# Kernel tuning notes

Measured on AMD Instinct MI355X. Metric: run time of the kernel, lower is better.

Reference implementation:

```python
import jax, jax.numpy as jnp
import numpy as np

NUM_HEADS = 16
HIDDEN = 1024
HEAD_DIM = HIDDEN // NUM_HEADS


def setup_inputs() -> dict:
    key = jax.random.key(0)
    ks = jax.random.split(key, 9)
    B, S = 2, 2048
    s = 1.0 / np.sqrt(HIDDEN)
    return {
        "x": jax.random.normal(ks[0], (B, S, HIDDEN), dtype=jnp.float32),
        "Wq": jax.random.normal(ks[1], (HIDDEN, HIDDEN), dtype=jnp.float32) * s,
        "bq": jnp.zeros((HIDDEN,), dtype=jnp.float32),
        "Wk": jax.random.normal(ks[2], (HIDDEN, HIDDEN), dtype=jnp.float32) * s,
        "bk": jnp.zeros((HIDDEN,), dtype=jnp.float32),
        "Wv": jax.random.normal(ks[3], (HIDDEN, HIDDEN), dtype=jnp.float32) * s,
        "bv": jnp.zeros((HIDDEN,), dtype=jnp.float32),
        "Wo": jax.random.normal(ks[4], (HIDDEN, HIDDEN), dtype=jnp.float32) * s,
        "bo": jnp.zeros((HIDDEN,), dtype=jnp.float32),
    }


def reference(x, Wq, bq, Wk, bk, Wv, bv, Wo, bo):
    B, S, H = x.shape
    # project and split heads: [B, S, H] -> [B, nh, S, hd]
    def split_heads(t):
        return t.reshape(B, S, NUM_HEADS, HEAD_DIM).transpose(0, 2, 1, 3)

    q = split_heads(x @ Wq + bq)
    k = split_heads(x @ Wk + bk)
    v = split_heads(x @ Wv + bv)

    scores = jnp.einsum("bhqd,bhkd->bhqk", q, k) / jnp.sqrt(
        jnp.asarray(HEAD_DIM, dtype=x.dtype))
    probs = jax.nn.softmax(scores, axis=-1)
    # attn_drop_rate = 0.0 -> dropout is identity
    ctx = jnp.einsum("bhqk,bhkd->bhqd", probs, v)
    ctx = ctx.transpose(0, 2, 1, 3).reshape(B, S, H)
    out = ctx @ Wo + bo
    return out
```

## Files before the change

### kernel.cpp

```cpp
#include <hip/hip_runtime.h>

#define NHEADS 16
#define HDIM   64
#define SEQL   2048
#define HID    1024
#define NB     2
#define MT     4096

#define QSCALE 0.18033688011112042f

typedef float        f4_t   __attribute__((ext_vector_type(4)));
typedef unsigned int u32x4  __attribute__((ext_vector_type(4)));
typedef __bf16       bf16x8 __attribute__((ext_vector_type(8)));

typedef const __attribute__((address_space(1))) unsigned int* gas_ptr;
typedef __attribute__((address_space(3))) unsigned int*       las_ptr;

__device__ __forceinline__ void gload16(const void* g, void* l){
  __builtin_amdgcn_global_load_lds((gas_ptr)g, (las_ptr)l, 16, 0, 0);
}
__device__ __forceinline__ unsigned int pkbf(float a, float b){
  unsigned short lo = __builtin_bit_cast(unsigned short, (__bf16)a);
  unsigned short hi = __builtin_bit_cast(unsigned short, (__bf16)b);
  return (unsigned)lo | ((unsigned)hi << 16);
}
__device__ __forceinline__ unsigned short f2bf(float f){
  return __builtin_bit_cast(unsigned short, (__bf16)f);
}
__device__ __forceinline__ u32x4 ld16(const unsigned short* p){
  return *reinterpret_cast<const u32x4*>(p);
}
__device__ __forceinline__ f4_t mfma_bf16(u32x4 a, u32x4 b, f4_t c){
  return __builtin_amdgcn_mfma_f32_16x16x32_bf16(
      __builtin_bit_cast(bf16x8, a), __builtin_bit_cast(bf16x8, b), c, 0, 0, 0);
}

__global__ __launch_bounds__(256) void xcast(const float* __restrict__ x,
                                             unsigned short* __restrict__ xb){
  int gid = blockIdx.x * 256 + threadIdx.x;
  float4 a = reinterpret_cast<const float4*>(x)[gid * 2];
  float4 b = reinterpret_cast<const float4*>(x)[gid * 2 + 1];
  u32x4 o;
  o[0] = pkbf(a.x, a.y);
  o[1] = pkbf(a.z, a.w);
  o[2] = pkbf(b.x, b.y);
  o[3] = pkbf(b.z, b.w);
  *reinterpret_cast<u32x4*>(&xb[gid * 8]) = o;
}

__global__ void prep_w(const float* __restrict__ Wq, const float* __restrict__ Wk,
                       const float* __restrict__ Wv, const float* __restrict__ Wo,
                       unsigned short* __restrict__ wqT, unsigned short* __restrict__ wkT,
                       unsigned short* __restrict__ wvT, unsigned short* __restrict__ woT){
  __shared__ float t[32][33];
  int z = blockIdx.z;
  const float* W = (z==0)?Wq:(z==1)?Wk:(z==2)?Wv:Wo;
  unsigned short* WT = (z==0)?wqT:(z==1)?wkT:(z==2)?wvT:woT;
  float sc = (z==0) ? QSCALE : 1.0f;
  int k0 = blockIdx.x*32, n0 = blockIdx.y*32;
  int tx = threadIdx.x, ty = threadIdx.y;
  #pragma unroll
  for (int ii=0; ii<4; ii++)
    t[ty+ii*8][tx] = W[(k0+ty+ii*8)*HID + n0+tx];
  __syncthreads();
  #pragma unroll
  for (int ii=0; ii<4; ii++)
    WT[(n0+ty+ii*8)*HID + k0+tx] = f2bf(t[tx][ty+ii*8] * sc);
}

__global__ __launch_bounds__(256) void qkv_gemm(
    const unsigned short* __restrict__ xb,
    const unsigned short* __restrict__ wqT, const unsigned short* __restrict__ wkT,
    const unsigned short* __restrict__ wvT,
    const float* __restrict__ bq, const float* __restrict__ bk, const float* __restrict__ bv,
    unsigned short* __restrict__ qo, unsigned short* __restrict__ ko,
    unsigned short* __restrict__ vto){
  __shared__ unsigned short As[128*32];
  __shared__ unsigned short Bs[128*32];
  const int z = blockIdx.z;
  const unsigned short* wT = (z==0)?wqT:(z==1)?wkT:wvT;
  const float* bias = (z==0)?bq:(z==1)?bk:bv;
  const float bscale = (z==0) ? QSCALE : 1.0f;
  const int m0 = blockIdx.x * 128;
  const int n0 = blockIdx.y * 128;
  const int tid = threadIdx.x;
  const int lane = tid & 63, w = tid >> 6;
  const int l15 = lane & 15, lg = lane >> 4;
  const int wr = (w >> 1) * 64, wc = (w & 1) * 64;
  const int srow = w*16 + (lane >> 2);
  const int skc  = (lane & 3) * 8;

  f4_t acc[4][4];
  f4_t z4 = {0.f, 0.f, 0.f, 0.f};
  #pragma unroll
  for (int i=0;i<4;i++)
    #pragma unroll
    for (int j=0;j<4;j++) acc[i][j] = z4;

  for (int kt = 0; kt < HID; kt += 32) {
    __syncthreads();
    #pragma unroll
    for (int c = 0; c < 2; c++) {
      int row = c*64 + srow;
      gload16(&xb[(m0+row)*HID + kt + skc], (char*)As + c*4096 + w*1024);
      gload16(&wT[(n0+row)*HID + kt + skc], (char*)Bs + c*4096 + w*1024);
    }
    __syncthreads();
    u32x4 a[4], b[4];
    #pragma unroll
    for (int i=0;i<4;i++) a[i] = ld16(&As[(wr + i*16 + l15)*32 + lg*8]);
    #pragma unroll
    for (int j=0;j<4;j++) b[j] = ld16(&Bs[(wc + j*16 + l15)*32 + lg*8]);
    #pragma unroll
    for (int i=0;i<4;i++)
      #pragma unroll
      for (int j=0;j<4;j++)
        acc[i][j] = mfma_bf16(a[i], b[j], acc[i][j]);
  }
  if (z == 2) {
    #pragma unroll
    for (int i=0;i<4;i++){
      int mrow = m0 + wr + i*16 + lg*4;
      int b_ = mrow >> 11, s = mrow & 2047;
      #pragma unroll
      for (int j=0;j<4;j++){
        int n = n0 + wc + j*16 + l15;
        float bs = bias[n];
        int h = n >> 6, d = n & 63;
        unsigned int lo = pkbf(acc[i][j][0]+bs, acc[i][j][1]+bs);
        unsigned int hi = pkbf(acc[i][j][2]+bs, acc[i][j][3]+bs);
        unsigned long long v8 = (unsigned long long)lo | ((unsigned long long)hi << 32);
        *reinterpret_cast<unsigned long long*>(
            vto + (((b_*NHEADS + h)*HDIM + d)*SEQL + s)) = v8;
      }
    }
  } else {
    unsigned short* outp = (z==0) ? qo : ko;
    #pragma unroll
    for (int i=0;i<4;i++){
      int mrow = m0 + wr + i*16 + lg*4;
      #pragma unroll
      for (int j=0;j<4;j++){
        int n = n0 + wc + j*16 + l15;
        float bs = bias[n] * bscale;
        int h = n >> 6, d = n & 63;
        #pragma unroll
        for (int r=0;r<4;r++){
          int m = mrow + r;
          int b_ = m >> 11, s = m & 2047;
          outp[(((b_*NHEADS + h)*SEQL) + s)*HDIM + d] = f2bf(acc[i][j][r] + bs);
        }
      }
    }
  }
}

__global__ __launch_bounds__(256) void flash(
    const unsigned short* __restrict__ q,
    const unsigned short* __restrict__ k,
    const unsigned short* __restrict__ vT,
    unsigned short* __restrict__ ctx){
  __shared__ unsigned short Ks[2][4096];
  __shared__ unsigned short Vs[2][4096];
  __shared__ unsigned short Ps[4][2048];
  const int bh = blockIdx.y;
  const int b_ = bh >> 4, h = bh & 15;
  const int tid = threadIdx.x;
  const int w = tid >> 6, lane = tid & 63;
  const int l15 = lane & 15, lg = lane >> 4;
  const int q0 = blockIdx.x*128 + w*32;
  const unsigned short* qb = q + (bh*SEQL + q0)*HDIM;
  const unsigned short* kp = k + bh*SEQL*HDIM;
  const unsigned short* vp = vT + bh*HDIM*SEQL;
  char* pw = (char*)Ps[w];
  const int swz = (l15 & 7) << 4;

  const int sr = w*16 + (lane >> 3);
  const int scol = ((lane & 7) ^ (sr & 7)) * 8;
  const int ldst = w*2048;

  u32x4 qf[2][2];
  #pragma unroll
  for (int qg=0; qg<2; qg++)
    #pragma unroll
    for (int ks=0; ks<2; ks++)
      qf[qg][ks] = ld16(&qb[(qg*16 + l15)*HDIM + ks*32 + lg*8]);

  float mr[2] = {-1e30f, -1e30f}, ls[2] = {0.f, 0.f};
  f4_t oacc[4][2];
  f4_t z4 = {0.f,0.f,0.f,0.f};
  #pragma unroll
  for (int dt=0;dt<4;dt++)
    #pragma unroll
    for (int qg=0;qg<2;qg++) oacc[dt][qg] = z4;

  auto stage = [&](int buf, int kb){
    const unsigned short* gk = kp + (kb + sr)*HDIM + scol;
    gload16(gk,           (char*)Ks[buf] + ldst);
    gload16(gk + 8*HDIM,  (char*)Ks[buf] + ldst + 1024);
    const unsigned short* gv = vp + sr*SEQL + kb + scol;
    gload16(gv,           (char*)Vs[buf] + ldst);
    gload16(gv + 8*SEQL,  (char*)Vs[buf] + ldst + 1024);
  };

  int cur = 0;
  stage(0, 0);
  __syncthreads();

  for (int kb = 0; kb < SEQL; kb += 64) {
    if (kb + 64 < SEQL) stage(cur^1, kb + 64);
    const char* kbase = (const char*)Ks[cur];
    const char* vbase = (const char*)Vs[cur];

    f4_t sacc[4][2];
    __builtin_amdgcn_s_setprio(1);
    #pragma unroll
    for (int t=0;t<4;t++){
      u32x4 k0 = *reinterpret_cast<const u32x4*>(kbase + (t*16+l15)*128 + ((lg*16) ^ swz));
      u32x4 k1 = *reinterpret_cast<const u32x4*>(kbase + (t*16+l15)*128 + ((64 + lg*16) ^ swz));
      #pragma unroll
      for (int qg=0;qg<2;qg++){
        f4_t s = mfma_bf16(k0, qf[qg][0], z4);
        sacc[t][qg] = mfma_bf16(k1, qf[qg][1], s);
      }
    }
    __builtin_amdgcn_s_setprio(0);

    float scl[2];
    #pragma unroll
    for (int qg=0;qg<2;qg++){
      float vm = sacc[0][qg][0];
      #pragma unroll
      for (int t=0;t<4;t++)
        #pragma unroll
        for (int r=0;r<4;r++) vm = fmaxf(vm, sacc[t][qg][r]);
      vm = fmaxf(vm, __shfl_xor(vm, 16));
      vm = fmaxf(vm, __shfl_xor(vm, 32));
      float mnew = fmaxf(mr[qg], vm);
      scl[qg] = exp2f(mr[qg] - mnew);
      mr[qg] = mnew;
      float ps = 0.f;
      #pragma unroll
      for (int t=0;t<4;t++)
        #pragma unroll
        for (int r=0;r<4;r++){
          float p = exp2f(sacc[t][qg][r] - mnew);
          sacc[t][qg][r] = p;
          ps += p;
        }
      ps += __shfl_xor(ps, 16);
      ps += __shfl_xor(ps, 32);
      ls[qg] = ls[qg]*scl[qg] + ps;
      int rowb = (qg*16 + l15)*128;
      #pragma unroll
      for (int t=0;t<4;t++){
        unsigned int lo = pkbf(sacc[t][qg][0], sacc[t][qg][1]);
        unsigned int hi = pkbf(sacc[t][qg][2], sacc[t][qg][3]);
        unsigned long long v8 = (unsigned long long)lo | ((unsigned long long)hi << 32);
        *reinterpret_cast<unsigned long long*>(pw + rowb + ((t*32 + lg*8) ^ swz)) = v8;
      }
    }
    #pragma unroll
    for (int dt=0;dt<4;dt++)
      #pragma unroll
      for (int qg=0;qg<2;qg++) oacc[dt][qg] *= scl[qg];

    u32x4 pf[2][2];
    #pragma unroll
    for (int qg=0;qg<2;qg++)
      #pragma unroll
      for (int ks=0;ks<2;ks++)
        pf[qg][ks] = *reinterpret_cast<const u32x4*>(
            pw + (qg*16 + l15)*128 + ((ks*64 + lg*16) ^ swz));

    __builtin_amdgcn_s_setprio(1);
    #pragma unroll
    for (int dt=0;dt<4;dt++){
      u32x4 v0 = *reinterpret_cast<const u32x4*>(vbase + (dt*16+l15)*128 + ((lg*16) ^ swz));
      u32x4 v1 = *reinterpret_cast<const u32x4*>(vbase + (dt*16+l15)*128 + ((64 + lg*16) ^ swz));
      #pragma unroll
      for (int qg=0;qg<2;qg++){
        f4_t o = mfma_bf16(v0, pf[qg][0], oacc[dt][qg]);
        oacc[dt][qg] = mfma_bf16(v1, pf[qg][1], o);
      }
    }
    __builtin_amdgcn_s_setprio(0);
    __syncthreads();
    cur ^= 1;
  }

  #pragma unroll
  for (int qg=0;qg<2;qg++){
    float inv = 1.0f / ls[qg];
    int orow = b_*SEQL + q0 + qg*16 + l15;
    unsigned short* cb = ctx + orow*HID + h*HDIM;
    #pragma unroll
    for (int dt=0;dt<4;dt++){
      unsigned int lo = pkbf(oacc[dt][qg][0]*inv, oacc[dt][qg][1]*inv);
      unsigned int hi = pkbf(oacc[dt][qg][2]*inv, oacc[dt][qg][3]*inv);
      unsigned long long v8 = (unsigned long long)lo | ((unsigned long long)hi << 32);
      *reinterpret_cast<unsigned long long*>(cb + dt*16 + lg*4) = v8;
    }
  }
}

__global__ __launch_bounds__(256) void out_gemm(
    const unsigned short* __restrict__ cb,
    const unsigned short* __restrict__ woT,
    const float* __restrict__ bo,
    float* __restrict__ out){
  __shared__ unsigned short As[128*32];
  __shared__ unsigned short Bs[128*32];
  const int m0 = blockIdx.x * 128;
  const int n0 = blockIdx.y * 128;
  const int tid = threadIdx.x;
  const int lane = tid & 63, w = tid >> 6;
  const int l15 = lane & 15, lg = lane >> 4;
  const int wr = (w >> 1) * 64, wc = (w & 1) * 64;
  const int srow = w*16 + (lane >> 2);
  const int skc  = (lane & 3) * 8;

  f4_t acc[4][4];
  f4_t z4 = {0.f,0.f,0.f,0.f};
  #pragma unroll
  for (int i=0;i<4;i++)
    #pragma unroll
    for (int j=0;j<4;j++) acc[i][j] = z4;

  for (int kt = 0; kt < HID; kt += 32) {
    __syncthreads();
    #pragma unroll
    for (int c = 0; c < 2; c++) {
      int row = c*64 + srow;
      gload16(&cb[(m0+row)*HID + kt + skc],  (char*)As + c*4096 + w*1024);
      gload16(&woT[(n0+row)*HID + kt + skc], (char*)Bs + c*4096 + w*1024);
    }
    __syncthreads();
    u32x4 a[4], b[4];
    #pragma unroll
    for (int i=0;i<4;i++) a[i] = ld16(&As[(wr + i*16 + l15)*32 + lg*8]);
    #pragma unroll
    for (int j=0;j<4;j++) b[j] = ld16(&Bs[(wc + j*16 + l15)*32 + lg*8]);
    #pragma unroll
    for (int i=0;i<4;i++)
      #pragma unroll
      for (int j=0;j<4;j++)
        acc[i][j] = mfma_bf16(a[i], b[j], acc[i][j]);
  }
  #pragma unroll
  for (int i=0;i<4;i++){
    int mrow = m0 + wr + i*16 + lg*4;
    #pragma unroll
    for (int j=0;j<4;j++){
      int n = n0 + wc + j*16 + l15;
      float bs = bo[n];
      #pragma unroll
      for (int r=0;r<4;r++)
        out[(mrow + r)*HID + n] = acc[i][j][r] + bs;
    }
  }
}

extern "C" void kernel_launch(void* const* d_in, const int* in_sizes, int n_in,
                              void* d_out, int out_size, void* d_ws, size_t ws_size,
                              hipStream_t stream){
  const float* x  = (const float*)d_in[0];
  const float* Wq = (const float*)d_in[1];
  const float* bq = (const float*)d_in[2];
  const float* Wk = (const float*)d_in[3];
  const float* bk = (const float*)d_in[4];
  const float* Wv = (const float*)d_in[5];
  const float* bv = (const float*)d_in[6];
  const float* Wo = (const float*)d_in[7];
  const float* bo = (const float*)d_in[8];
  float* out = (float*)d_out;

  char* ws = (char*)d_ws;
  size_t off = 0;
  auto alloc = [&](size_t bytes) -> void* {
    void* p = ws + off;
    off += (bytes + 255) & ~(size_t)255;
    return p;
  };
  unsigned short* xb   = (unsigned short*)alloc((size_t)MT*HID*2);
  unsigned short* wqT  = (unsigned short*)alloc((size_t)HID*HID*2);
  unsigned short* wkT  = (unsigned short*)alloc((size_t)HID*HID*2);
  unsigned short* wvT  = (unsigned short*)alloc((size_t)HID*HID*2);
  unsigned short* woT  = (unsigned short*)alloc((size_t)HID*HID*2);
  unsigned short* q_ws = (unsigned short*)alloc((size_t)MT*HID*2);
  unsigned short* k_ws = (unsigned short*)alloc((size_t)MT*HID*2);
  unsigned short* vT_ws= (unsigned short*)alloc((size_t)MT*HID*2);
  unsigned short* c_ws = (unsigned short*)alloc((size_t)MT*HID*2);

  prep_w<<<dim3(32,32,4), dim3(32,8), 0, stream>>>(Wq,Wk,Wv,Wo, wqT,wkT,wvT,woT);
  xcast<<<dim3(2048), dim3(256), 0, stream>>>(x, xb);
  qkv_gemm<<<dim3(32,8,3), dim3(256), 0, stream>>>(xb, wqT,wkT,wvT, bq,bk,bv,
                                                   q_ws, k_ws, vT_ws);
  flash<<<dim3(16,32), dim3(256), 0, stream>>>(q_ws, k_ws, vT_ws, c_ws);
  out_gemm<<<dim3(32,8), dim3(256), 0, stream>>>(c_ws, woT, bo, out);
}
```

Before: 177.8 us.

## Split flash attention across 8 waves with 16 rows each and lazy rescaling

The flash kernel now runs 512 threads per block, and each of 8 waves handles 16 query rows instead of 4 waves handling 32. That halves per-wave registers and accumulators and shares the K/V staging across more waves. It also adds a conditional online-softmax rescale: the running max and accumulators are only updated when a wave-wide new max exceeds the old one by more than a threshold. This trades exp and multiply work for more waves contending at each barrier, and risks larger exp values in bf16 P when rescaling is skipped.

```diff
diff --git a/kernel.cpp b/kernel.cpp
--- a/kernel.cpp
+++ b/kernel.cpp
@@ -8,6 +8,7 @@
 #define MT     4096
 
 #define QSCALE 0.18033688011112042f
+#define RESCALE_THR 6.0f
 
 typedef float        f4_t   __attribute__((ext_vector_type(4)));
 typedef unsigned int u32x4  __attribute__((ext_vector_type(4)));
@@ -155,52 +156,44 @@
   }
 }
 
-__global__ __launch_bounds__(256) void flash(
+__global__ __launch_bounds__(512) void flash(
     const unsigned short* __restrict__ q,
     const unsigned short* __restrict__ k,
     const unsigned short* __restrict__ vT,
     unsigned short* __restrict__ ctx){
   __shared__ unsigned short Ks[2][4096];
   __shared__ unsigned short Vs[2][4096];
-  __shared__ unsigned short Ps[4][2048];
+  __shared__ unsigned short Ps[8][1024];
   const int bh = blockIdx.y;
   const int b_ = bh >> 4, h = bh & 15;
   const int tid = threadIdx.x;
   const int w = tid >> 6, lane = tid & 63;
   const int l15 = lane & 15, lg = lane >> 4;
-  const int q0 = blockIdx.x*128 + w*32;
+  const int q0 = blockIdx.x*128 + w*16;
   const unsigned short* qb = q + (bh*SEQL + q0)*HDIM;
   const unsigned short* kp = k + bh*SEQL*HDIM;
   const unsigned short* vp = vT + bh*HDIM*SEQL;
   char* pw = (char*)Ps[w];
   const int swz = (l15 & 7) << 4;
 
-  const int sr = w*16 + (lane >> 3);
+  const int sr = w*8 + (lane >> 3);
   const int scol = ((lane & 7) ^ (sr & 7)) * 8;
-  const int ldst = w*2048;
-
-  u32x4 qf[2][2];
-  #pragma unroll
-  for (int qg=0; qg<2; qg++)
-    #pragma unroll
-    for (int ks=0; ks<2; ks++)
-      qf[qg][ks] = ld16(&qb[(qg*16 + l15)*HDIM + ks*32 + lg*8]);
-
-  float mr[2] = {-1e30f, -1e30f}, ls[2] = {0.f, 0.f};
-  f4_t oacc[4][2];
+  const int ldst = w*1024;
+
+  u32x4 qf[2];
+  #pragma unroll
+  for (int ks=0; ks<2; ks++)
+    qf[ks] = ld16(&qb[l15*HDIM + ks*32 + lg*8]);
+
+  float mr = -1e30f, ls = 0.f;
+  f4_t oacc[4];
   f4_t z4 = {0.f,0.f,0.f,0.f};
   #pragma unroll
-  for (int dt=0;dt<4;dt++)
-    #pragma unroll
-    for (int qg=0;qg<2;qg++) oacc[dt][qg] = z4;
+  for (int dt=0;dt<4;dt++) oacc[dt] = z4;
 
   auto stage = [&](int buf, int kb){
-    const unsigned short* gk = kp + (kb + sr)*HDIM + scol;
-    gload16(gk,           (char*)Ks[buf] + ldst);
-    gload16(gk + 8*HDIM,  (char*)Ks[buf] + ldst + 1024);
-    const unsigned short* gv = vp + sr*SEQL + kb + scol;
-    gload16(gv,           (char*)Vs[buf] + ldst);
-    gload16(gv + 8*SEQL,  (char*)Vs[buf] + ldst + 1024);
+    gload16(kp + (kb + sr)*HDIM + scol, (char*)Ks[buf] + ldst);
+    gload16(vp + sr*SEQL + kb + scol,   (char*)Vs[buf] + ldst);
   };
 
   int cur = 0;
@@ -212,95 +205,82 @@
     const char* kbase = (const char*)Ks[cur];
     const char* vbase = (const char*)Vs[cur];
 
-    f4_t sacc[4][2];
+    f4_t sacc[4];
     __builtin_amdgcn_s_setprio(1);
     #pragma unroll
     for (int t=0;t<4;t++){
       u32x4 k0 = *reinterpret_cast<const u32x4*>(kbase + (t*16+l15)*128 + ((lg*16) ^ swz));
       u32x4 k1 = *reinterpret_cast<const u32x4*>(kbase + (t*16+l15)*128 + ((64 + lg*16) ^ swz));
-      #pragma unroll
-      for (int qg=0;qg<2;qg++){
-        f4_t s = mfma_bf16(k0, qf[qg][0], z4);
-        sacc[t][qg] = mfma_bf16(k1, qf[qg][1], s);
+      f4_t s = mfma_bf16(k0, qf[0], z4);
+      sacc[t] = mfma_bf16(k1, qf[1], s);
+    }
+    __builtin_amdgcn_s_setprio(0);
+
+    float vm = sacc[0][0];
+    #pragma unroll
+    for (int t=0;t<4;t++)
+      #pragma unroll
+      for (int r=0;r<4;r++) vm = fmaxf(vm, sacc[t][r]);
+    vm = fmaxf(vm, __shfl_xor(vm, 16));
+    vm = fmaxf(vm, __shfl_xor(vm, 32));
+    if (!__all(vm - mr <= RESCALE_THR)) {
+      float mnew = fmaxf(mr, vm);
+      float scl = exp2f(mr - mnew);
+      mr = mnew;
+      ls *= scl;
+      #pragma unroll
+      for (int dt=0;dt<4;dt++) oacc[dt] *= scl;
+    }
+    float ps = 0.f;
+    #pragma unroll
+    for (int t=0;t<4;t++)
+      #pragma unroll
+      for (int r=0;r<4;r++){
+        float p = exp2f(sacc[t][r] - mr);
+        sacc[t][r] = p;
+        ps += p;
       }
-    }
-    __builtin_amdgcn_s_setprio(0);
-
-    float scl[2];
-    #pragma unroll
-    for (int qg=0;qg<2;qg++){
-      float vm = sacc[0][qg][0];
-      #pragma unroll
-      for (int t=0;t<4;t++)
-        #pragma unroll
-        for (int r=0;r<4;r++) vm = fmaxf(vm, sacc[t][qg][r]);
-      vm = fmaxf(vm, __shfl_xor(vm, 16));
-      vm = fmaxf(vm, __shfl_xor(vm, 32));
-      float mnew = fmaxf(mr[qg], vm);
-      scl[qg] = exp2f(mr[qg] - mnew);
-      mr[qg] = mnew;
-      float ps = 0.f;
-      #pragma unroll
-      for (int t=0;t<4;t++)
-        #pragma unroll
-        for (int r=0;r<4;r++){
-          float p = exp2f(sacc[t][qg][r] - mnew);
-          sacc[t][qg][r] = p;
-          ps += p;
-        }
-      ps += __shfl_xor(ps, 16);
-      ps += __shfl_xor(ps, 32);
-      ls[qg] = ls[qg]*scl[qg] + ps;
-      int rowb = (qg*16 + l15)*128;
+    ps += __shfl_xor(ps, 16);
+    ps += __shfl_xor(ps, 32);
+    ls += ps;
+    {
+      int rowb = l15*128;
       #pragma unroll
       for (int t=0;t<4;t++){
-        unsigned int lo = pkbf(sacc[t][qg][0], sacc[t][qg][1]);
-        unsigned int hi = pkbf(sacc[t][qg][2], sacc[t][qg][3]);
+        unsigned int lo = pkbf(sacc[t][0], sacc[t][1]);
+        unsigned int hi = pkbf(sacc[t][2], sacc[t][3]);
         unsigned long long v8 = (unsigned long long)lo | ((unsigned long long)hi << 32);
         *reinterpret_cast<unsigned long long*>(pw + rowb + ((t*32 + lg*8) ^ swz)) = v8;
       }
     }
-    #pragma unroll
-    for (int dt=0;dt<4;dt++)
-      #pragma unroll
-      for (int qg=0;qg<2;qg++) oacc[dt][qg] *= scl[qg];
-
-    u32x4 pf[2][2];
-    #pragma unroll
-    for (int qg=0;qg<2;qg++)
-      #pragma unroll
-      for (int ks=0;ks<2;ks++)
-        pf[qg][ks] = *reinterpret_cast<const u32x4*>(
-            pw + (qg*16 + l15)*128 + ((ks*64 + lg*16) ^ swz));
+    u32x4 pf[2];
+    #pragma unroll
+    for (int ks=0;ks<2;ks++)
+      pf[ks] = *reinterpret_cast<const u32x4*>(
+          pw + l15*128 + ((ks*64 + lg*16) ^ swz));
 
     __builtin_amdgcn_s_setprio(1);
     #pragma unroll
     for (int dt=0;dt<4;dt++){
       u32x4 v0 = *reinterpret_cast<const u32x4*>(vbase + (dt*16+l15)*128 + ((lg*16) ^ swz));
       u32x4 v1 = *reinterpret_cast<const u32x4*>(vbase + (dt*16+l15)*128 + ((64 + lg*16) ^ swz));
-      #pragma unroll
-      for (int qg=0;qg<2;qg++){
-        f4_t o = mfma_bf16(v0, pf[qg][0], oacc[dt][qg]);
-        oacc[dt][qg] = mfma_bf16(v1, pf[qg][1], o);
-      }
+      f4_t o = mfma_bf16(v0, pf[0], oacc[dt]);
+      oacc[dt] = mfma_bf16(v1, pf[1], o);
     }
     __builtin_amdgcn_s_setprio(0);
     __syncthreads();
     cur ^= 1;
   }
 
-  #pragma unroll
-  for (int qg=0;qg<2;qg++){
-    float inv = 1.0f / ls[qg];
-    int orow = b_*SEQL + q0 + qg*16 + l15;
-    unsigned short* cb = ctx + orow*HID + h*HDIM;
-    #pragma unroll
-    for (int dt=0;dt<4;dt++){
-      unsigned int lo = pkbf(oacc[dt][qg][0]*inv, oacc[dt][qg][1]*inv);
-      unsigned int hi = pkbf(oacc[dt][qg][2]*inv, oacc[dt][qg][3]*inv);
-      unsigned long long v8 = (unsigned long long)lo | ((unsigned long long)hi << 32);
-      *reinterpret_cast<unsigned long long*>(cb + dt*16 + lg*4) = v8;
-    }
+  float inv = 1.0f / ls;
+  int orow = b_*SEQL + q0 + l15;
+  unsigned short* cb = ctx + orow*HID + h*HDIM;
+  #pragma unroll
+  for (int dt=0;dt<4;dt++){
+    unsigned int lo = pkbf(oacc[dt][0]*inv, oacc[dt][1]*inv);
+    unsigned int hi = pkbf(oacc[dt][2]*inv, oacc[dt][3]*inv);
+    unsigned long long v8 = (unsigned long long)lo | ((unsigned long long)hi << 32);
+    *reinterpret_cast<unsigned long long*>(cb + dt*16 + lg*4) = v8;
   }
 }
 
@@ -396,6 +376,6 @@
   xcast<<<dim3(2048), dim3(256), 0, stream>>>(x, xb);
   qkv_gemm<<<dim3(32,8,3), dim3(256), 0, stream>>>(xb, wqT,wkT,wvT, bq,bk,bv,
                                                    q_ws, k_ws, vT_ws);
-  flash<<<dim3(16,32), dim3(256), 0, stream>>>(q_ws, k_ws, vT_ws, c_ws);
+  flash<<<dim3(16,32), dim3(512), 0, stream>>>(q_ws, k_ws, vT_ws, c_ws);
   out_gemm<<<dim3(32,8), dim3(256), 0, stream>>>(c_ws, woT, bo, out);
 }
```

Measured after the change: 163.4 us. -8.1%, faster.
